# Kernel optimization log

Hardware: AMD Instinct MI355X
Metric: run time of the kernel (lower is better)

The kernel has to match this reference:

```python
import jax, jax.numpy as jnp
import numpy as np

# ---- static config (eval-mode RPN, torchvision-style FPN) ----
LEVEL_HW = [(200, 200), (100, 100), (50, 50), (25, 25), (13, 13)]
STRIDES = [4, 8, 16, 32, 64]
SIZES = [32, 64, 128, 256, 512]
A = 3                      # anchors per location (3 aspect ratios)
IMG_H, IMG_W = 800, 800
PRE_N, POST_N = 1000, 1000 # pre/post NMS top-n (testing)
NMS_TH, SCORE_TH, MIN_SIZE = 0.7, 0.0, 1e-3
BBOX_CLIP = 4.135166556742356  # log(1000/16), BoxCoder clamp
NUM_PER_LEVEL = [A * h * w for h, w in LEVEL_HW]


def _make_anchors():
    ratios = np.array([0.5, 1.0, 2.0])
    hr = np.sqrt(ratios)
    wr = 1.0 / hr
    out = []
    for (H, W), size, stride in zip(LEVEL_HW, SIZES, STRIDES):
        ws, hs = wr * size, hr * size
        base = np.stack([-ws / 2, -hs / 2, ws / 2, hs / 2], axis=1)  # [A,4]
        sx = np.arange(W) * stride
        sy = np.arange(H) * stride
        yy, xx = np.meshgrid(sy, sx, indexing='ij')
        shifts = np.stack([xx.ravel(), yy.ravel(), xx.ravel(), yy.ravel()], axis=1)
        out.append((shifts[:, None, :] + base[None, :, :]).reshape(-1, 4))
    return np.concatenate(out, 0).astype(np.float32)


def setup_inputs() -> dict:
    key = jax.random.key(0)
    ks = jax.random.split(key, 10)
    N = 4
    inp = {}
    for i, (h, w) in enumerate(LEVEL_HW):
        inp[f'obj{i}'] = jax.random.normal(ks[i], (N, A, h, w), jnp.float32)
        inp[f'delta{i}'] = 0.5 * jax.random.normal(ks[5 + i], (N, 4 * A, h, w), jnp.float32)
    inp['anchors'] = jnp.asarray(_make_anchors())
    return inp


def _decode(deltas, anchors):
    # BoxCoder.decode with weights (1,1,1,1)
    wa = anchors[:, 2] - anchors[:, 0]
    ha = anchors[:, 3] - anchors[:, 1]
    cxa = anchors[:, 0] + 0.5 * wa
    cya = anchors[:, 1] + 0.5 * ha
    dx, dy = deltas[..., 0], deltas[..., 1]
    dw = jnp.minimum(deltas[..., 2], BBOX_CLIP)
    dh = jnp.minimum(deltas[..., 3], BBOX_CLIP)
    cx = dx * wa + cxa
    cy = dy * ha + cya
    w = jnp.exp(dw) * wa
    h = jnp.exp(dh) * ha
    return jnp.stack([cx - 0.5 * w, cy - 0.5 * h, cx + 0.5 * w, cy + 0.5 * h], -1)


def _box_iou(b1, b2):
    a1 = (b1[:, 2] - b1[:, 0]) * (b1[:, 3] - b1[:, 1])
    a2 = (b2[:, 2] - b2[:, 0]) * (b2[:, 3] - b2[:, 1])
    lt = jnp.maximum(b1[:, None, :2], b2[None, :, :2])
    rb = jnp.minimum(b1[:, None, 2:], b2[None, :, 2:])
    wh = jnp.clip(rb - lt, 0.0)
    inter = wh[..., 0] * wh[..., 1]
    return inter / (a1[:, None] + a2[None, :] - inter)


def _nms_keep(iou, valid):
    # greedy NMS over score-sorted boxes; valid marks surviving pre-filters
    K = iou.shape[0]
    def body(sup, i):
        k = valid[i] & jnp.logical_not(sup[i])
        sup = sup | (k & (iou[i] > NMS_TH))
        return sup, k
    _, keeps = jax.lax.scan(body, jnp.zeros(K, bool), jnp.arange(K))
    return keeps


def _per_image(boxes, scores, lvl):
    # clip_boxes_to_image
    x1 = jnp.clip(boxes[:, 0], 0.0, IMG_W)
    y1 = jnp.clip(boxes[:, 1], 0.0, IMG_H)
    x2 = jnp.clip(boxes[:, 2], 0.0, IMG_W)
    y2 = jnp.clip(boxes[:, 3], 0.0, IMG_H)
    boxes = jnp.stack([x1, y1, x2, y2], -1)
    # remove_small_boxes + score_thresh as validity mask
    valid = (x2 - x1 >= MIN_SIZE) & (y2 - y1 >= MIN_SIZE) & (scores >= SCORE_TH)
    ms = jnp.where(valid, scores, -1.0)
    order = jnp.argsort(-ms)
    b_s, v_s, s_s, l_s = boxes[order], valid[order], scores[order], lvl[order]
    # batched_nms trick: offset boxes by level so levels never overlap
    bn = jax.lax.stop_gradient(b_s) + (l_s.astype(boxes.dtype) * (IMG_W + 1.0))[:, None]
    keep = _nms_keep(_box_iou(bn, bn), v_s)
    sel_key = jnp.where(keep, jax.lax.stop_gradient(s_s), -1.0)
    topv, topi = jax.lax.top_k(sel_key, POST_N)
    m = topv > -0.5
    fb = jnp.where(m[:, None], b_s[topi], 0.0)
    fs = jnp.where(m, s_s[topi], 0.0)
    return fb, fs


def reference(obj0, obj1, obj2, obj3, obj4, delta0, delta1, delta2, delta3, delta4, anchors):
    objs = [obj0, obj1, obj2, obj3, obj4]
    dels = [delta0, delta1, delta2, delta3, delta4]
    N = obj0.shape[0]
    # permute_and_flatten + concat (objectness C=1)
    obj = jnp.concatenate([o.transpose(0, 2, 3, 1).reshape(N, -1) for o in objs], 1)
    dl = jnp.concatenate([
        d.reshape(N, A, 4, d.shape[2], d.shape[3]).transpose(0, 3, 4, 1, 2).reshape(N, -1, 4)
        for d in dels], 1)
    proposals = _decode(dl, anchors)  # [N, total, 4]
    levels = jnp.concatenate([jnp.full((n,), i, jnp.int32) for i, n in enumerate(NUM_PER_LEVEL)])
    # per-level top-k (static split)
    idxs, off = [], 0
    for n in NUM_PER_LEVEL:
        k = min(PRE_N, n)
        _, ti = jax.lax.top_k(obj[:, off:off + n], k)
        idxs.append(ti + off)
        off += n
    top_idx = jnp.concatenate(idxs, 1)  # [N, K]
    sel_obj = jnp.take_along_axis(obj, top_idx, 1)
    sel_lvl = levels[top_idx]
    sel_box = jnp.take_along_axis(proposals, top_idx[..., None], 1)
    scores = jax.nn.sigmoid(sel_obj)
    fb, fs = jax.vmap(_per_image)(sel_box, scores, sel_lvl)
    return fb, fs
```

## Files before the change

kernel.cpp:

```cpp
#include <hip/hip_runtime.h>
#include <cstdint>
#include <cstddef>

#define NLV 5
#define NIMG 4
#define NSEL 4507
#define TSEL (NIMG * NSEL)
#define POSTN 1000
#define TCAP 8192
#define TTCAP 2048
#define NHB 16
#define PBLK 64
#define PCH 1875

__device__ const int d_W[NLV]    = {200, 100, 50, 25, 13};
__device__ const int d_NL[NLV]   = {120000, 30000, 7500, 1875, 507};
__device__ const int d_KOFF[6]   = {0, 120000, 150000, 157500, 159375, 159882};
__device__ const int d_LOFF[6]   = {0, 1000, 2000, 3000, 4000, 4507};
__device__ const int d_KL[NLV]   = {1000, 1000, 1000, 1000, 507};

struct Ptrs {
    const float* obj[NLV];
    const float* del[NLV];
    const float* anch;
};

__device__ inline unsigned int dkey_of(float f) {
    unsigned int u = __float_as_uint(f);
    unsigned int mk = (u & 0x80000000u) ? ~u : (u | 0x80000000u);
    return ~mk;
}
__device__ inline float logit_from_dkey(unsigned int dk) {
    unsigned int mk = ~dk;
    unsigned int u = (mk & 0x80000000u) ? (mk & 0x7fffffffu) : ~mk;
    return __uint_as_float(u);
}

__global__ __launch_bounds__(256) void k_hist(Ptrs P, unsigned int* hist) {
    int l = blockIdx.y, n = blockIdx.z;
    int nl_sz = d_NL[l];
    if (d_KL[l] >= nl_sz) return;
    int nlid = n * NLV + l;
    __shared__ unsigned int h[2048];
    for (int i = threadIdx.x; i < 2048; i += 256) h[i] = 0;
    __syncthreads();
    const float* ob = P.obj[l] + (size_t)n * nl_sz;
    int chunk = (nl_sz + NHB - 1) / NHB;
    int beg = blockIdx.x * chunk;
    int end = min(beg + chunk, nl_sz);
    for (int t = beg + (int)threadIdx.x; t < end; t += 256)
        atomicAdd(&h[dkey_of(ob[t]) >> 21], 1u);
    __syncthreads();
    unsigned int* out = hist + ((size_t)nlid * NHB + blockIdx.x) * 2048;
    for (int i = threadIdx.x; i < 2048; i += 256) out[i] = h[i];
}

__global__ __launch_bounds__(1024) void k_thresh(const unsigned int* hist,
                                                 unsigned int* thr,
                                                 int* scnt, int* tcnt) {
    int nlid = blockIdx.x;
    int l = nlid % NLV;
    if (threadIdx.x == 0) { scnt[nlid] = 0; tcnt[nlid] = 0; }
    if (d_KL[l] >= d_NL[l]) return;
    int tid = threadIdx.x, w = tid >> 6, lane = tid & 63;
    __shared__ unsigned int wpre[16];
    const unsigned int* hb = hist + (size_t)nlid * NHB * 2048;
    unsigned int v0 = 0, v1 = 0;
    #pragma unroll
    for (int sh = 0; sh < NHB; ++sh) {
        v0 += hb[sh * 2048 + 2 * tid];
        v1 += hb[sh * 2048 + 2 * tid + 1];
    }
    unsigned int s = v0 + v1;
    unsigned int ps = s;
    #pragma unroll
    for (int d = 1; d < 64; d <<= 1) {
        unsigned int t2 = (unsigned int)__shfl_up((int)ps, d, 64);
        if (lane >= d) ps += t2;
    }
    if (lane == 63) wpre[w] = ps;
    __syncthreads();
    unsigned int base = 0;
    #pragma unroll
    for (int ww = 0; ww < 16; ++ww) if (ww < w) base += wpre[ww];
    unsigned int incl = base + ps;
    unsigned int target = (unsigned int)d_KL[l];
    unsigned int exc0 = incl - s, inc0 = incl - v1;
    unsigned int exc1 = inc0,    inc1 = incl;
    if (exc0 < target && target <= inc0) { thr[nlid * 2] = 2 * tid;     thr[nlid * 2 + 1] = exc0; }
    if (exc1 < target && target <= inc1) { thr[nlid * 2] = 2 * tid + 1; thr[nlid * 2 + 1] = exc1; }
}

__global__ __launch_bounds__(256) void k_pick(Ptrs P, const unsigned int* thr,
                                              int* scnt, int* tcnt,
                                              int* cg, float* cl,
                                              unsigned long long* tiebuf) {
    int l = blockIdx.y, n = blockIdx.z;
    int nl_sz = d_NL[l], kl = d_KL[l];
    int nlid = n * NLV + l;
    const float* ob = P.obj[l] + (size_t)n * nl_sz;
    int cbase = n * NSEL + d_LOFF[l];
    int koff = d_KOFF[l];
    int Wl = d_W[l], HW = Wl * Wl;
    int chunk = (nl_sz + PBLK - 1) / PBLK;
    int beg = blockIdx.x * chunk;
    int end = min(beg + chunk, nl_sz);
    int tid = threadIdx.x;

    if (kl >= nl_sz) {
        for (int t = beg + tid; t < end; t += 256) {
            int a = t / HW, rem = t - a * HW;
            int p = rem * 3 + a;
            cg[cbase + p] = koff + p;
            cl[cbase + p] = ob[t];
        }
        return;
    }
    __shared__ int sp[PCH];
    __shared__ float sl[PCH];
    __shared__ unsigned long long tb[PCH];
    __shared__ int nsel, ntie, sbase, tbase;
    if (tid == 0) { nsel = 0; ntie = 0; }
    __syncthreads();

    unsigned int b0 = thr[nlid * 2];
    for (int t = beg + tid; t < end; t += 256) {
        float lg = ob[t];
        unsigned int dk = dkey_of(lg);
        unsigned int bin = dk >> 21;
        if (bin < b0) {
            int pos = atomicAdd(&nsel, 1);
            int a = t / HW, rem = t - a * HW;
            sp[pos] = rem * 3 + a;
            sl[pos] = lg;
        } else if (bin == b0) {
            int pos = atomicAdd(&ntie, 1);
            int a = t / HW, rem = t - a * HW;
            tb[pos] = ((unsigned long long)dk << 17) |
                      (unsigned long long)(unsigned int)(rem * 3 + a);
        }
    }
    __syncthreads();
    if (tid == 0) {
        sbase = atomicAdd(&scnt[nlid], nsel);
        tbase = atomicAdd(&tcnt[nlid], ntie);
    }
    __syncthreads();
    int ns = nsel, nt = ntie, sb = sbase, tbs = tbase;
    for (int i = tid; i < ns; i += 256) {
        cg[cbase + sb + i] = koff + sp[i];
        cl[cbase + sb + i] = sl[i];
    }
    for (int i = tid; i < nt; i += 256) {
        int slot = tbs + i;
        if (slot < TCAP) tiebuf[(size_t)nlid * TCAP + slot] = tb[i];
    }
}

__global__ __launch_bounds__(1024) void k_tie(const unsigned int* thr, const int* tcnt,
                                              const unsigned long long* tiebuf,
                                              int* cg, float* cl) {
    int nlid = blockIdx.x;
    int n = nlid / NLV, l = nlid % NLV;
    if (d_KL[l] >= d_NL[l]) return;
    __shared__ unsigned long long kk[TCAP];
    __shared__ unsigned long long tt[TTCAP];
    __shared__ unsigned int h2[2048];
    __shared__ unsigned int wpre[16];
    __shared__ unsigned int s_b1, s_before;
    __shared__ int ctr, ttc;
    int c = min(tcnt[nlid], TCAP);
    unsigned int cnt_lt = thr[nlid * 2 + 1];
    int need = d_KL[l] - (int)cnt_lt;
    int tid = threadIdx.x, w = tid >> 6, lane = tid & 63;
    if (tid == 0) { ctr = 0; ttc = 0; }
    h2[tid] = 0; h2[tid + 1024] = 0;
    for (int i = tid; i < c; i += 1024) kk[i] = tiebuf[(size_t)nlid * TCAP + i];
    __syncthreads();
    for (int i = tid; i < c; i += 1024)
        atomicAdd(&h2[(unsigned int)((kk[i] >> 27) & 0x7ffull)], 1u);
    __syncthreads();
    unsigned int v0 = h2[2 * tid], v1 = h2[2 * tid + 1];
    unsigned int s = v0 + v1, ps = s;
    #pragma unroll
    for (int d = 1; d < 64; d <<= 1) {
        unsigned int t2 = (unsigned int)__shfl_up((int)ps, d, 64);
        if (lane >= d) ps += t2;
    }
    if (lane == 63) wpre[w] = ps;
    __syncthreads();
    unsigned int base = 0;
    #pragma unroll
    for (int ww = 0; ww < 16; ++ww) if (ww < w) base += wpre[ww];
    unsigned int incl = base + ps;
    unsigned int target = (unsigned int)need;
    unsigned int exc0 = incl - s, inc0 = incl - v1;
    unsigned int exc1 = inc0,    inc1 = incl;
    if (exc0 < target && target <= inc0) { s_b1 = 2 * tid;     s_before = exc0; }
    if (exc1 < target && target <= inc1) { s_b1 = 2 * tid + 1; s_before = exc1; }
    __syncthreads();
    unsigned int b1 = s_b1;
    int before = (int)s_before;
    int cbase = n * NSEL + d_LOFF[l];
    int koff = d_KOFF[l];
    for (int i = tid; i < c; i += 1024) {
        unsigned long long ki = kk[i];
        unsigned int sb = (unsigned int)((ki >> 27) & 0x7ffull);
        if (sb < b1) {
            int slot = atomicAdd(&ctr, 1);
            int p = (int)(ki & 0x1ffffull);
            cg[cbase + (int)cnt_lt + slot] = koff + p;
            cl[cbase + (int)cnt_lt + slot] = logit_from_dkey((unsigned int)(ki >> 17));
        } else if (sb == b1) {
            int j = atomicAdd(&ttc, 1);
            if (j < TTCAP) tt[j] = ki;
        }
    }
    __syncthreads();
    int c2 = min(ttc, TTCAP);
    int need2 = need - before;
    for (int i = tid; i < c2; i += 1024) {
        unsigned long long ki = tt[i];
        int rank = 0;
        for (int j = 0; j < c2; ++j) rank += (tt[j] < ki) ? 1 : 0;
        if (rank < need2) {
            int p = (int)(ki & 0x1ffffull);
            cg[cbase + (int)cnt_lt + before + rank] = koff + p;
            cl[cbase + (int)cnt_lt + before + rank] = logit_from_dkey((unsigned int)(ki >> 17));
        }
    }
}

__global__ __launch_bounds__(256) void k_build(Ptrs P, const int* cg, const float* cl,
                                               unsigned long long* pkey,
                                               float4* pbox, float4* pbn, float* plog) {
#pragma clang fp contract(off)
    int t = blockIdx.x * blockDim.x + threadIdx.x;
    if (t >= NIMG * NLV * 1024) return;
    int nl = t >> 10, j = t & 1023;
    int n = nl / NLV, l = nl % NLV;
    if (j >= d_KL[l]) {
        pkey[t] = ((unsigned long long)0xFFFFFFFFu << 27) | (unsigned long long)j;
        pbox[t] = make_float4(0.f, 0.f, 0.f, 0.f);
        pbn[t]  = make_float4(0.f, 0.f, 0.f, 0.f);
        plog[t] = 0.f;
        return;
    }
    int s = n * NSEL + d_LOFF[l] + j;
    int gidx = cg[s];
    float lg = cl[s];
    int p = gidx - d_KOFF[l];
    int Wl = d_W[l];
    int HW = Wl * Wl;
    int a = p % 3, hw = p / 3;
    int h = hw / Wl, w = hw - h * Wl;
    const float* dl = P.del[l];
    size_t base = (size_t)(n * 12 + a * 4) * HW + (size_t)h * Wl + w;
    float dx = dl[base], dy = dl[base + HW];
    float dw = dl[base + 2 * (size_t)HW], dh = dl[base + 3 * (size_t)HW];
    const float* an = P.anch + 4 * (size_t)gidx;
    float ax1 = an[0], ay1 = an[1], ax2 = an[2], ay2 = an[3];
    float wa = ax2 - ax1, ha = ay2 - ay1;
    float cxa = ax1 + 0.5f * wa, cya = ay1 + 0.5f * ha;
    const float CLIPC = (float)4.135166556742356;
    dw = fminf(dw, CLIPC); dh = fminf(dh, CLIPC);
    float cx = dx * wa + cxa;
    float cy = dy * ha + cya;
    float ww = expf(dw) * wa;
    float hh = expf(dh) * ha;
    float x1 = cx - 0.5f * ww, y1 = cy - 0.5f * hh;
    float x2 = cx + 0.5f * ww, y2 = cy + 0.5f * hh;
    x1 = fminf(fmaxf(x1, 0.0f), 800.0f);
    y1 = fminf(fmaxf(y1, 0.0f), 800.0f);
    x2 = fminf(fmaxf(x2, 0.0f), 800.0f);
    y2 = fminf(fmaxf(y2, 0.0f), 800.0f);
    bool valid = (x2 - x1 >= 1e-3f) && (y2 - y1 >= 1e-3f);
    float off = (float)l * 801.0f;
    pbox[t] = make_float4(x1, y1, x2, y2);
    pbn[t]  = make_float4(x1 + off, y1 + off, x2 + off, y2 + off);
    plog[t] = lg;
    unsigned int sk = valid ? dkey_of(lg) : 0xffffffffu;
    pkey[t] = ((unsigned long long)sk << 27) |
              ((unsigned long long)(unsigned int)p << 10) | (unsigned long long)j;
}

__global__ __launch_bounds__(512) void k_sortL(const unsigned long long* pkey,
                                               const float4* pbox, const float4* pbn,
                                               const float* plog,
                                               unsigned long long* skey,
                                               float4* sboxL, float4* cboxL, float* slogL,
                                               int* ccnt) {
    __shared__ unsigned long long s[1024];
    int nl = blockIdx.x, tid = threadIdx.x;
    s[tid] = pkey[nl * 1024 + tid];
    s[tid + 512] = pkey[nl * 1024 + tid + 512];
    __syncthreads();
    for (int k = 2; k <= 1024; k <<= 1) {
        for (int j = k >> 1; j > 0; j >>= 1) {
            int i = ((tid & ~(j - 1)) << 1) | (tid & (j - 1));
            int ix = i | j;
            bool up = ((i & k) == 0);
            unsigned long long A = s[i], B = s[ix];
            if ((A > B) == up) { s[i] = B; s[ix] = A; }
            __syncthreads();
        }
    }
    for (int e = tid; e < 1024; e += 512) {
        unsigned long long key = s[e];
        int j = (int)(key & 0x3ffull);
        int src = nl * 1024 + j;
        skey[nl * 1024 + e] = key;
        sboxL[nl * 1024 + e] = pbox[src];
        cboxL[nl * 1024 + e] = pbn[src];
        slogL[nl * 1024 + e] = plog[src];
        bool v = (key >> 27) != 0xFFFFFFFFull;
        bool vn = (e < 1023) ? ((s[e + 1] >> 27) != 0xFFFFFFFFull) : false;
        if (e == 0 && !v) ccnt[nl] = 0;
        if (v && (e == 1023 || !vn)) ccnt[nl] = e + 1;
    }
}

__global__ __launch_bounds__(256) void k_mask(const float4* cboxL, const int* ccnt,
                                              unsigned long long* MT) {
#pragma clang fp contract(off)
    int n = blockIdx.z, l = blockIdx.y;
    int ci = blockIdx.x >> 4, cj = blockIdx.x & 15;
    int nl = n * NLV + l;
    int cnt = ccnt[nl];
    int nw = (cnt + 63) / 64;
    if (cj < ci || cj >= nw) return;
    __shared__ float4 bi[64], bj[64];
    int tid = threadIdx.x;
    if (tid < 64) bj[tid] = cboxL[nl * 1024 + cj * 64 + tid];
    else if (tid < 128) bi[tid - 64] = cboxL[nl * 1024 + ci * 64 + (tid - 64)];
    __syncthreads();
    int w = tid >> 6, lane = tid & 63;
    float4 B = bj[lane];
    float a2 = (B.z - B.x) * (B.w - B.y);
    unsigned long long* outp = MT + ((size_t)nl * 16 + cj) * 1024 + ci * 64;
    #pragma unroll
    for (int t = 0; t < 16; ++t) {
        int i = w * 16 + t;
        float4 A = bi[i];
        float a1 = (A.z - A.x) * (A.w - A.y);
        float ltx = fmaxf(A.x, B.x), lty = fmaxf(A.y, B.y);
        float rbx = fminf(A.z, B.z), rby = fminf(A.w, B.w);
        float wx = fmaxf(rbx - ltx, 0.f), wy = fmaxf(rby - lty, 0.f);
        float inter = wx * wy;
        float iou = inter / ((a1 + a2) - inter);
        unsigned long long word = __ballot(iou > 0.7f);
        if (lane == 0) outp[i] = word;
    }
}

__global__ __launch_bounds__(1024) void k_scan(const unsigned long long* MT,
                                               const int* ccnt,
                                               unsigned long long* keepL) {
    int l = blockIdx.x, n = blockIdx.y;
    int nl = n * NLV + l;
    int tid = threadIdx.x, w = tid >> 6, lane = tid & 63;
    __shared__ unsigned long long pendS[16];
    __shared__ unsigned long long defS[16];
    int cnt = ccnt[nl];
    int nw = (cnt + 63) / 64;

    const unsigned long long* base = MT + ((size_t)nl * 16 + w) * 1024;
    unsigned long long Dmask = 0;
    if (w < nw)
        Dmask = base[(size_t)w * 64 + lane] & ~((2ull << lane) - 1ull);
    unsigned long long rows[15];
    #pragma unroll
    for (int cc = 0; cc < 15; ++cc)
        rows[cc] = (cc < w && w < nw) ? base[(size_t)cc * 64 + lane] : 0ull;

    int nb = max(0, min(64, cnt - w * 64));
    unsigned long long pend_w = (nb == 64) ? ~0ull : ((nb > 0) ? ((1ull << nb) - 1ull) : 0ull);
    unsigned long long K_w = 0;
    if (lane == 0) pendS[w] = pend_w;
    __syncthreads();

    for (int round = 0; round < 1024; ++round) {
        unsigned long long any = 0;
        #pragma unroll
        for (int cc = 0; cc < 16; ++cc) any |= pendS[cc];
        if (!any) break;
        unsigned long long acc = ((pendS[w] >> lane) & 1ull) ? Dmask : 0ull;
        #pragma unroll
        for (int cc = 0; cc < 15; ++cc)
            if (cc < w) acc |= ((pendS[cc] >> lane) & 1ull) ? rows[cc] : 0ull;
        unsigned int vlo = (unsigned int)acc, vhi = (unsigned int)(acc >> 32);
        #pragma unroll
        for (int m = 1; m < 64; m <<= 1) {
            vlo |= (unsigned int)__shfl_xor((int)vlo, m, 64);
            vhi |= (unsigned int)__shfl_xor((int)vhi, m, 64);
        }
        unsigned long long sup = ((unsigned long long)vhi << 32) | (unsigned long long)vlo;
        unsigned long long def_w = pend_w & ~sup;
        K_w |= def_w;
        if (lane == 0) defS[w] = def_w;
        __syncthreads();
        unsigned long long acc2 = ((defS[w] >> lane) & 1ull) ? Dmask : 0ull;
        #pragma unroll
        for (int cc = 0; cc < 15; ++cc)
            if (cc < w) acc2 |= ((defS[cc] >> lane) & 1ull) ? rows[cc] : 0ull;
        unsigned int rlo = (unsigned int)acc2, rhi = (unsigned int)(acc2 >> 32);
        #pragma unroll
        for (int m = 1; m < 64; m <<= 1) {
            rlo |= (unsigned int)__shfl_xor((int)rlo, m, 64);
            rhi |= (unsigned int)__shfl_xor((int)rhi, m, 64);
        }
        unsigned long long rem = ((unsigned long long)rhi << 32) | (unsigned long long)rlo;
        pend_w &= ~def_w & ~rem;
        if (lane == 0) pendS[w] = pend_w;
        __syncthreads();
    }
    if (lane == 0) keepL[nl * 16 + w] = K_w;
}

__global__ __launch_bounds__(1024) void k_rank(const unsigned long long* skey,
                                               const unsigned long long* keepL,
                                               const int* ccnt,
                                               const float4* sboxL, const float* slogL,
                                               float* out) {
    int n = blockIdx.x, tid = threadIdx.x;
    __shared__ unsigned long long KS[NLV][1024];
    __shared__ unsigned long long kd[NLV][16];
    __shared__ int kpre[NLV][17];
    __shared__ int lcnt[NLV];
    for (int i = tid; i < POSTN; i += 1024) {
        ((float4*)out)[n * POSTN + i] = make_float4(0.f, 0.f, 0.f, 0.f);
        out[NIMG * POSTN * 4 + n * POSTN + i] = 0.f;
    }
    for (int e = tid; e < NLV * 1024; e += 1024)
        ((unsigned long long*)KS)[e] = skey[(size_t)n * NLV * 1024 + e];
    if (tid < NLV * 16) ((unsigned long long*)kd)[tid] = keepL[n * NLV * 16 + tid];
    if (tid < NLV) lcnt[tid] = ccnt[n * NLV + tid];
    __syncthreads();
    if (tid < NLV) {
        int run = 0;
        for (int q = 0; q < 16; ++q) { kpre[tid][q] = run; run += (int)__popcll(kd[tid][q]); }
        kpre[tid][16] = run;
    }
    __syncthreads();
    for (int e = tid; e < NLV * 1024; e += 1024) {
        int l = e >> 10, i = e & 1023;
        if (i >= lcnt[l]) continue;
        int q = i >> 6, b = i & 63;
        if (!((kd[l][q] >> b) & 1ull)) continue;
        int rank = kpre[l][q] + (int)__popcll(kd[l][q] & ((1ull << b) - 1ull));
        unsigned int sk = (unsigned int)(KS[l][i] >> 27);
        for (int l2 = 0; l2 < NLV; ++l2) {
            if (l2 == l) continue;
            int c2 = lcnt[l2];
            unsigned long long bound = (l2 < l)
                ? (((unsigned long long)sk + 1ull) << 27)
                : ((unsigned long long)sk << 27);
            int lo = 0, hi = c2;
            while (lo < hi) {
                int mid = (lo + hi) >> 1;
                if (KS[l2][mid] < bound) lo = mid + 1; else hi = mid;
            }
            int mq = lo >> 6, mb = lo & 63;
            rank += kpre[l2][mq] + (mb ? (int)__popcll(kd[l2][mq] & ((1ull << mb) - 1ull)) : 0);
        }
        if (rank < POSTN) {
            ((float4*)out)[n * POSTN + rank] = sboxL[(size_t)(n * NLV + l) * 1024 + i];
            float lg = slogL[(size_t)(n * NLV + l) * 1024 + i];
            out[NIMG * POSTN * 4 + n * POSTN + rank] = 1.0f / (1.0f + expf(-lg));
        }
    }
}

extern "C" void kernel_launch(void* const* d_in, const int* in_sizes, int n_in,
                              void* d_out, int out_size, void* d_ws, size_t ws_size,
                              hipStream_t stream) {
    Ptrs P;
    bool interleaved = (in_sizes[1] == 4 * in_sizes[0]);
    for (int i = 0; i < NLV; ++i) {
        if (interleaved) {
            P.obj[i] = (const float*)d_in[2 * i];
            P.del[i] = (const float*)d_in[2 * i + 1];
        } else {
            P.obj[i] = (const float*)d_in[i];
            P.del[i] = (const float*)d_in[NLV + i];
        }
    }
    P.anch = (const float*)d_in[10];

    char* w = (char*)d_ws;
    size_t off = 0;
    auto alloc = [&](size_t bytes) {
        void* p = w + off;
        off = (off + bytes + 255) & ~(size_t)255;
        return p;
    };
    const size_t NLT = (size_t)NIMG * NLV * 1024;
    unsigned int* hist = (unsigned int*)alloc((size_t)NIMG * NLV * NHB * 2048 * 4);
    int* scnt = (int*)alloc(256);
    int* tcnt = (int*)alloc(256);
    unsigned int* thr = (unsigned int*)alloc((size_t)NIMG * NLV * 2 * 4);
    unsigned long long* tiebuf = (unsigned long long*)alloc((size_t)NIMG * NLV * TCAP * 8);
    int* cg      = (int*)alloc((size_t)TSEL * 4);
    float* cl    = (float*)alloc((size_t)TSEL * 4);
    unsigned long long* pkey = (unsigned long long*)alloc(NLT * 8);
    float4* pbox = (float4*)alloc(NLT * 16);
    float4* pbn  = (float4*)alloc(NLT * 16);
    float* plog  = (float*)alloc(NLT * 4);
    unsigned long long* skey = (unsigned long long*)alloc(NLT * 8);
    float4* sboxL = (float4*)alloc(NLT * 16);
    float4* cboxL = (float4*)alloc(NLT * 16);
    float* slogL  = (float*)alloc(NLT * 4);
    int* ccnt    = (int*)alloc((size_t)NIMG * NLV * 4);
    unsigned long long* keepL = (unsigned long long*)alloc((size_t)NIMG * NLV * 16 * 8);
    unsigned long long* MT = (unsigned long long*)alloc((size_t)NIMG * NLV * 16 * 1024 * 8);
    (void)ws_size; (void)n_in;

    k_hist<<<dim3(NHB, NLV, NIMG), 256, 0, stream>>>(P, hist);
    k_thresh<<<NIMG * NLV, 1024, 0, stream>>>(hist, thr, scnt, tcnt);
    k_pick<<<dim3(PBLK, NLV, NIMG), 256, 0, stream>>>(P, thr, scnt, tcnt, cg, cl, tiebuf);
    k_tie<<<NIMG * NLV, 1024, 0, stream>>>(thr, tcnt, tiebuf, cg, cl);
    k_build<<<(NIMG * NLV * 1024) / 256, 256, 0, stream>>>(P, cg, cl, pkey, pbox, pbn, plog);
    k_sortL<<<NIMG * NLV, 512, 0, stream>>>(pkey, pbox, pbn, plog, skey, sboxL, cboxL, slogL, ccnt);
    k_mask<<<dim3(256, NLV, NIMG), 256, 0, stream>>>(cboxL, ccnt, MT);
    k_scan<<<dim3(NLV, NIMG), 1024, 0, stream>>>(MT, ccnt, keepL);
    k_rank<<<NIMG, 1024, 0, stream>>>(skey, keepL, ccnt, sboxL, slogL, (float*)d_out);
}
```

Measured before the change: 172.3 us.

## Fuse histogram with threshold and merge tie/build/sort/mask/scan into one kernel

Merges the per-chunk histogram and threshold kernels into a single 1024-thread block per image-level that builds the histogram in shared memory, using sub-histograms to reduce atomic contention. Folds tie resolution, box decode, bitonic sort, the IoU mask and the NMS scan into one mega-kernel per image-level, keeping intermediates in a shared-memory union instead of global buffers. This removes several launches and global round-trips. In exchange the histogram pass now runs on only 20 blocks, one reading 120k elements, and the IoU mask uses 16 waves per block instead of many blocks, which lowers parallelism.

```diff
diff --git a/kernel.cpp b/kernel.cpp
--- a/kernel.cpp
+++ b/kernel.cpp
@@ -9,9 +9,10 @@
 #define POSTN 1000
 #define TCAP 8192
 #define TTCAP 2048
-#define NHB 16
 #define PBLK 64
 #define PCH 1875
+#define NSUB 4
+#define NTRI 136
 
 __device__ const int d_W[NLV]    = {200, 100, 50, 25, 13};
 __device__ const int d_NL[NLV]   = {120000, 30000, 7500, 1875, 507};
@@ -36,40 +37,29 @@
     return __uint_as_float(u);
 }
 
-__global__ __launch_bounds__(256) void k_hist(Ptrs P, unsigned int* hist) {
-    int l = blockIdx.y, n = blockIdx.z;
+__global__ __launch_bounds__(1024) void k_histthresh(Ptrs P, unsigned int* thr,
+                                                     int* scnt, int* tcnt) {
+    int nlid = blockIdx.x;
+    int n = nlid / NLV, l = nlid % NLV;
+    int tid = threadIdx.x;
+    if (tid == 0) { scnt[nlid] = 0; tcnt[nlid] = 0; }
+    if (d_KL[l] >= d_NL[l]) return;
+    __shared__ unsigned int h[NSUB][2048];
+    __shared__ unsigned int wpre[16];
+    for (int i = tid; i < NSUB * 2048; i += 1024) (&h[0][0])[i] = 0;
+    __syncthreads();
     int nl_sz = d_NL[l];
-    if (d_KL[l] >= nl_sz) return;
-    int nlid = n * NLV + l;
-    __shared__ unsigned int h[2048];
-    for (int i = threadIdx.x; i < 2048; i += 256) h[i] = 0;
-    __syncthreads();
     const float* ob = P.obj[l] + (size_t)n * nl_sz;
-    int chunk = (nl_sz + NHB - 1) / NHB;
-    int beg = blockIdx.x * chunk;
-    int end = min(beg + chunk, nl_sz);
-    for (int t = beg + (int)threadIdx.x; t < end; t += 256)
-        atomicAdd(&h[dkey_of(ob[t]) >> 21], 1u);
-    __syncthreads();
-    unsigned int* out = hist + ((size_t)nlid * NHB + blockIdx.x) * 2048;
-    for (int i = threadIdx.x; i < 2048; i += 256) out[i] = h[i];
-}
-
-__global__ __launch_bounds__(1024) void k_thresh(const unsigned int* hist,
-                                                 unsigned int* thr,
-                                                 int* scnt, int* tcnt) {
-    int nlid = blockIdx.x;
-    int l = nlid % NLV;
-    if (threadIdx.x == 0) { scnt[nlid] = 0; tcnt[nlid] = 0; }
-    if (d_KL[l] >= d_NL[l]) return;
-    int tid = threadIdx.x, w = tid >> 6, lane = tid & 63;
-    __shared__ unsigned int wpre[16];
-    const unsigned int* hb = hist + (size_t)nlid * NHB * 2048;
+    unsigned int* hs = h[(tid >> 8) & (NSUB - 1)];
+    for (int t = tid; t < nl_sz; t += 1024)
+        atomicAdd(&hs[dkey_of(ob[t]) >> 21], 1u);
+    __syncthreads();
+    int w = tid >> 6, lane = tid & 63;
     unsigned int v0 = 0, v1 = 0;
     #pragma unroll
-    for (int sh = 0; sh < NHB; ++sh) {
-        v0 += hb[sh * 2048 + 2 * tid];
-        v1 += hb[sh * 2048 + 2 * tid + 1];
+    for (int sh = 0; sh < NSUB; ++sh) {
+        v0 += h[sh][2 * tid];
+        v1 += h[sh][2 * tid + 1];
     }
     unsigned int s = v0 + v1;
     unsigned int ps = s;
@@ -157,264 +147,265 @@
     }
 }
 
-__global__ __launch_bounds__(1024) void k_tie(const unsigned int* thr, const int* tcnt,
-                                              const unsigned long long* tiebuf,
-                                              int* cg, float* cl) {
-    int nlid = blockIdx.x;
-    int n = nlid / NLV, l = nlid % NLV;
-    if (d_KL[l] >= d_NL[l]) return;
-    __shared__ unsigned long long kk[TCAP];
-    __shared__ unsigned long long tt[TTCAP];
-    __shared__ unsigned int h2[2048];
+__global__ __launch_bounds__(1024) void k_mega(Ptrs P, const unsigned int* thr,
+                                               const int* tcnt,
+                                               const unsigned long long* tiebuf,
+                                               int* cg, float* cl,
+                                               unsigned long long* skey,
+                                               float4* sboxL, float* slogL,
+                                               int* ccnt, unsigned long long* keepL) {
+#pragma clang fp contract(off)
+    __shared__ union {
+        struct { unsigned long long kk[TCAP];
+                 unsigned long long tt[TTCAP];
+                 unsigned int h2[2048]; } tie;
+        struct { unsigned long long s[1024];
+                 float4 bx[1024];
+                 float4 bn[1024];
+                 float lg[1024]; } srt;
+        struct { unsigned long long tri[NTRI * 64];
+                 float4 bb[1024]; } nms;
+    } U;
     __shared__ unsigned int wpre[16];
     __shared__ unsigned int s_b1, s_before;
-    __shared__ int ctr, ttc;
-    int c = min(tcnt[nlid], TCAP);
-    unsigned int cnt_lt = thr[nlid * 2 + 1];
-    int need = d_KL[l] - (int)cnt_lt;
-    int tid = threadIdx.x, w = tid >> 6, lane = tid & 63;
-    if (tid == 0) { ctr = 0; ttc = 0; }
-    h2[tid] = 0; h2[tid + 1024] = 0;
-    for (int i = tid; i < c; i += 1024) kk[i] = tiebuf[(size_t)nlid * TCAP + i];
-    __syncthreads();
-    for (int i = tid; i < c; i += 1024)
-        atomicAdd(&h2[(unsigned int)((kk[i] >> 27) & 0x7ffull)], 1u);
-    __syncthreads();
-    unsigned int v0 = h2[2 * tid], v1 = h2[2 * tid + 1];
-    unsigned int s = v0 + v1, ps = s;
-    #pragma unroll
-    for (int d = 1; d < 64; d <<= 1) {
-        unsigned int t2 = (unsigned int)__shfl_up((int)ps, d, 64);
-        if (lane >= d) ps += t2;
-    }
-    if (lane == 63) wpre[w] = ps;
-    __syncthreads();
-    unsigned int base = 0;
-    #pragma unroll
-    for (int ww = 0; ww < 16; ++ww) if (ww < w) base += wpre[ww];
-    unsigned int incl = base + ps;
-    unsigned int target = (unsigned int)need;
-    unsigned int exc0 = incl - s, inc0 = incl - v1;
-    unsigned int exc1 = inc0,    inc1 = incl;
-    if (exc0 < target && target <= inc0) { s_b1 = 2 * tid;     s_before = exc0; }
-    if (exc1 < target && target <= inc1) { s_b1 = 2 * tid + 1; s_before = exc1; }
-    __syncthreads();
-    unsigned int b1 = s_b1;
-    int before = (int)s_before;
-    int cbase = n * NSEL + d_LOFF[l];
-    int koff = d_KOFF[l];
-    for (int i = tid; i < c; i += 1024) {
-        unsigned long long ki = kk[i];
-        unsigned int sb = (unsigned int)((ki >> 27) & 0x7ffull);
-        if (sb < b1) {
-            int slot = atomicAdd(&ctr, 1);
-            int p = (int)(ki & 0x1ffffull);
-            cg[cbase + (int)cnt_lt + slot] = koff + p;
-            cl[cbase + (int)cnt_lt + slot] = logit_from_dkey((unsigned int)(ki >> 17));
-        } else if (sb == b1) {
-            int j = atomicAdd(&ttc, 1);
-            if (j < TTCAP) tt[j] = ki;
-        }
-    }
-    __syncthreads();
-    int c2 = min(ttc, TTCAP);
-    int need2 = need - before;
-    for (int i = tid; i < c2; i += 1024) {
-        unsigned long long ki = tt[i];
-        int rank = 0;
-        for (int j = 0; j < c2; ++j) rank += (tt[j] < ki) ? 1 : 0;
-        if (rank < need2) {
-            int p = (int)(ki & 0x1ffffull);
-            cg[cbase + (int)cnt_lt + before + rank] = koff + p;
-            cl[cbase + (int)cnt_lt + before + rank] = logit_from_dkey((unsigned int)(ki >> 17));
-        }
-    }
-}
-
-__global__ __launch_bounds__(256) void k_build(Ptrs P, const int* cg, const float* cl,
-                                               unsigned long long* pkey,
-                                               float4* pbox, float4* pbn, float* plog) {
-#pragma clang fp contract(off)
-    int t = blockIdx.x * blockDim.x + threadIdx.x;
-    if (t >= NIMG * NLV * 1024) return;
-    int nl = t >> 10, j = t & 1023;
-    int n = nl / NLV, l = nl % NLV;
-    if (j >= d_KL[l]) {
-        pkey[t] = ((unsigned long long)0xFFFFFFFFu << 27) | (unsigned long long)j;
-        pbox[t] = make_float4(0.f, 0.f, 0.f, 0.f);
-        pbn[t]  = make_float4(0.f, 0.f, 0.f, 0.f);
-        plog[t] = 0.f;
-        return;
-    }
-    int s = n * NSEL + d_LOFF[l] + j;
-    int gidx = cg[s];
-    float lg = cl[s];
-    int p = gidx - d_KOFF[l];
-    int Wl = d_W[l];
-    int HW = Wl * Wl;
-    int a = p % 3, hw = p / 3;
-    int h = hw / Wl, w = hw - h * Wl;
-    const float* dl = P.del[l];
-    size_t base = (size_t)(n * 12 + a * 4) * HW + (size_t)h * Wl + w;
-    float dx = dl[base], dy = dl[base + HW];
-    float dw = dl[base + 2 * (size_t)HW], dh = dl[base + 3 * (size_t)HW];
-    const float* an = P.anch + 4 * (size_t)gidx;
-    float ax1 = an[0], ay1 = an[1], ax2 = an[2], ay2 = an[3];
-    float wa = ax2 - ax1, ha = ay2 - ay1;
-    float cxa = ax1 + 0.5f * wa, cya = ay1 + 0.5f * ha;
-    const float CLIPC = (float)4.135166556742356;
-    dw = fminf(dw, CLIPC); dh = fminf(dh, CLIPC);
-    float cx = dx * wa + cxa;
-    float cy = dy * ha + cya;
-    float ww = expf(dw) * wa;
-    float hh = expf(dh) * ha;
-    float x1 = cx - 0.5f * ww, y1 = cy - 0.5f * hh;
-    float x2 = cx + 0.5f * ww, y2 = cy + 0.5f * hh;
-    x1 = fminf(fmaxf(x1, 0.0f), 800.0f);
-    y1 = fminf(fmaxf(y1, 0.0f), 800.0f);
-    x2 = fminf(fmaxf(x2, 0.0f), 800.0f);
-    y2 = fminf(fmaxf(y2, 0.0f), 800.0f);
-    bool valid = (x2 - x1 >= 1e-3f) && (y2 - y1 >= 1e-3f);
-    float off = (float)l * 801.0f;
-    pbox[t] = make_float4(x1, y1, x2, y2);
-    pbn[t]  = make_float4(x1 + off, y1 + off, x2 + off, y2 + off);
-    plog[t] = lg;
-    unsigned int sk = valid ? dkey_of(lg) : 0xffffffffu;
-    pkey[t] = ((unsigned long long)sk << 27) |
-              ((unsigned long long)(unsigned int)p << 10) | (unsigned long long)j;
-}
-
-__global__ __launch_bounds__(512) void k_sortL(const unsigned long long* pkey,
-                                               const float4* pbox, const float4* pbn,
-                                               const float* plog,
-                                               unsigned long long* skey,
-                                               float4* sboxL, float4* cboxL, float* slogL,
-                                               int* ccnt) {
-    __shared__ unsigned long long s[1024];
-    int nl = blockIdx.x, tid = threadIdx.x;
-    s[tid] = pkey[nl * 1024 + tid];
-    s[tid + 512] = pkey[nl * 1024 + tid + 512];
-    __syncthreads();
-    for (int k = 2; k <= 1024; k <<= 1) {
-        for (int j = k >> 1; j > 0; j >>= 1) {
-            int i = ((tid & ~(j - 1)) << 1) | (tid & (j - 1));
-            int ix = i | j;
-            bool up = ((i & k) == 0);
-            unsigned long long A = s[i], B = s[ix];
-            if ((A > B) == up) { s[i] = B; s[ix] = A; }
-            __syncthreads();
-        }
-    }
-    for (int e = tid; e < 1024; e += 512) {
-        unsigned long long key = s[e];
-        int j = (int)(key & 0x3ffull);
-        int src = nl * 1024 + j;
-        skey[nl * 1024 + e] = key;
-        sboxL[nl * 1024 + e] = pbox[src];
-        cboxL[nl * 1024 + e] = pbn[src];
-        slogL[nl * 1024 + e] = plog[src];
-        bool v = (key >> 27) != 0xFFFFFFFFull;
-        bool vn = (e < 1023) ? ((s[e + 1] >> 27) != 0xFFFFFFFFull) : false;
-        if (e == 0 && !v) ccnt[nl] = 0;
-        if (v && (e == 1023 || !vn)) ccnt[nl] = e + 1;
-    }
-}
-
-__global__ __launch_bounds__(256) void k_mask(const float4* cboxL, const int* ccnt,
-                                              unsigned long long* MT) {
-#pragma clang fp contract(off)
-    int n = blockIdx.z, l = blockIdx.y;
-    int ci = blockIdx.x >> 4, cj = blockIdx.x & 15;
-    int nl = n * NLV + l;
-    int cnt = ccnt[nl];
-    int nw = (cnt + 63) / 64;
-    if (cj < ci || cj >= nw) return;
-    __shared__ float4 bi[64], bj[64];
-    int tid = threadIdx.x;
-    if (tid < 64) bj[tid] = cboxL[nl * 1024 + cj * 64 + tid];
-    else if (tid < 128) bi[tid - 64] = cboxL[nl * 1024 + ci * 64 + (tid - 64)];
-    __syncthreads();
-    int w = tid >> 6, lane = tid & 63;
-    float4 B = bj[lane];
-    float a2 = (B.z - B.x) * (B.w - B.y);
-    unsigned long long* outp = MT + ((size_t)nl * 16 + cj) * 1024 + ci * 64;
-    #pragma unroll
-    for (int t = 0; t < 16; ++t) {
-        int i = w * 16 + t;
-        float4 A = bi[i];
-        float a1 = (A.z - A.x) * (A.w - A.y);
-        float ltx = fmaxf(A.x, B.x), lty = fmaxf(A.y, B.y);
-        float rbx = fminf(A.z, B.z), rby = fminf(A.w, B.w);
-        float wx = fmaxf(rbx - ltx, 0.f), wy = fmaxf(rby - lty, 0.f);
-        float inter = wx * wy;
-        float iou = inter / ((a1 + a2) - inter);
-        unsigned long long word = __ballot(iou > 0.7f);
-        if (lane == 0) outp[i] = word;
-    }
-}
-
-__global__ __launch_bounds__(1024) void k_scan(const unsigned long long* MT,
-                                               const int* ccnt,
-                                               unsigned long long* keepL) {
+    __shared__ int ctr, ttc, s_cnt;
+    __shared__ unsigned long long pendS[16];
+    __shared__ unsigned long long defS[16];
+
     int l = blockIdx.x, n = blockIdx.y;
     int nl = n * NLV + l;
     int tid = threadIdx.x, w = tid >> 6, lane = tid & 63;
-    __shared__ unsigned long long pendS[16];
-    __shared__ unsigned long long defS[16];
-    int cnt = ccnt[nl];
-    int nw = (cnt + 63) / 64;
-
-    const unsigned long long* base = MT + ((size_t)nl * 16 + w) * 1024;
-    unsigned long long Dmask = 0;
-    if (w < nw)
-        Dmask = base[(size_t)w * 64 + lane] & ~((2ull << lane) - 1ull);
-    unsigned long long rows[15];
-    #pragma unroll
-    for (int cc = 0; cc < 15; ++cc)
-        rows[cc] = (cc < w && w < nw) ? base[(size_t)cc * 64 + lane] : 0ull;
-
-    int nb = max(0, min(64, cnt - w * 64));
-    unsigned long long pend_w = (nb == 64) ? ~0ull : ((nb > 0) ? ((1ull << nb) - 1ull) : 0ull);
-    unsigned long long K_w = 0;
-    if (lane == 0) pendS[w] = pend_w;
-    __syncthreads();
-
-    for (int round = 0; round < 1024; ++round) {
-        unsigned long long any = 0;
+    int kl = d_KL[l], nl_sz = d_NL[l];
+    int cbase = n * NSEL + d_LOFF[l];
+    int koff = d_KOFF[l];
+
+    if (kl < nl_sz) {
+        int c = min(tcnt[nl], TCAP);
+        unsigned int cnt_lt = thr[nl * 2 + 1];
+        int need = kl - (int)cnt_lt;
+        if (tid == 0) { ctr = 0; ttc = 0; }
+        U.tie.h2[tid] = 0; U.tie.h2[tid + 1024] = 0;
+        for (int i = tid; i < c; i += 1024) U.tie.kk[i] = tiebuf[(size_t)nl * TCAP + i];
+        __syncthreads();
+        for (int i = tid; i < c; i += 1024)
+            atomicAdd(&U.tie.h2[(unsigned int)((U.tie.kk[i] >> 27) & 0x7ffull)], 1u);
+        __syncthreads();
+        unsigned int v0 = U.tie.h2[2 * tid], v1 = U.tie.h2[2 * tid + 1];
+        unsigned int s = v0 + v1, ps = s;
         #pragma unroll
-        for (int cc = 0; cc < 16; ++cc) any |= pendS[cc];
-        if (!any) break;
-        unsigned long long acc = ((pendS[w] >> lane) & 1ull) ? Dmask : 0ull;
+        for (int d = 1; d < 64; d <<= 1) {
+            unsigned int t2 = (unsigned int)__shfl_up((int)ps, d, 64);
+            if (lane >= d) ps += t2;
+        }
+        if (lane == 63) wpre[w] = ps;
+        __syncthreads();
+        unsigned int base = 0;
+        #pragma unroll
+        for (int ww = 0; ww < 16; ++ww) if (ww < w) base += wpre[ww];
+        unsigned int incl = base + ps;
+        unsigned int target = (unsigned int)need;
+        unsigned int exc0 = incl - s, inc0 = incl - v1;
+        unsigned int exc1 = inc0,    inc1 = incl;
+        if (exc0 < target && target <= inc0) { s_b1 = 2 * tid;     s_before = exc0; }
+        if (exc1 < target && target <= inc1) { s_b1 = 2 * tid + 1; s_before = exc1; }
+        __syncthreads();
+        unsigned int b1 = s_b1;
+        int before = (int)s_before;
+        for (int i = tid; i < c; i += 1024) {
+            unsigned long long ki = U.tie.kk[i];
+            unsigned int sb = (unsigned int)((ki >> 27) & 0x7ffull);
+            if (sb < b1) {
+                int slot = atomicAdd(&ctr, 1);
+                int p = (int)(ki & 0x1ffffull);
+                cg[cbase + (int)cnt_lt + slot] = koff + p;
+                cl[cbase + (int)cnt_lt + slot] = logit_from_dkey((unsigned int)(ki >> 17));
+            } else if (sb == b1) {
+                int j = atomicAdd(&ttc, 1);
+                if (j < TTCAP) U.tie.tt[j] = ki;
+            }
+        }
+        __syncthreads();
+        int c2 = min(ttc, TTCAP);
+        int need2 = need - before;
+        for (int i = tid; i < c2; i += 1024) {
+            unsigned long long ki = U.tie.tt[i];
+            int rank = 0;
+            for (int j = 0; j < c2; ++j) rank += (U.tie.tt[j] < ki) ? 1 : 0;
+            if (rank < need2) {
+                int p = (int)(ki & 0x1ffffull);
+                cg[cbase + (int)cnt_lt + before + rank] = koff + p;
+                cl[cbase + (int)cnt_lt + before + rank] = logit_from_dkey((unsigned int)(ki >> 17));
+            }
+        }
+    }
+    __syncthreads();
+
+    {
+        int j = tid;
+        unsigned long long key;
+        float4 box, bnv;
+        float lgv;
+        if (j >= kl) {
+            key = ((unsigned long long)0xFFFFFFFFu << 27) | (unsigned long long)j;
+            box = make_float4(0.f, 0.f, 0.f, 0.f);
+            bnv = box;
+            lgv = 0.f;
+        } else {
+            int sidx = cbase + j;
+            int gidx = cg[sidx];
+            float lg = cl[sidx];
+            int p = gidx - koff;
+            int Wl = d_W[l];
+            int HW = Wl * Wl;
+            int a = p % 3, hw = p / 3;
+            int hq = hw / Wl, wq = hw - hq * Wl;
+            const float* dl = P.del[l];
+            size_t dbase = (size_t)(n * 12 + a * 4) * HW + (size_t)hq * Wl + wq;
+            float dx = dl[dbase], dy = dl[dbase + HW];
+            float dw = dl[dbase + 2 * (size_t)HW], dh = dl[dbase + 3 * (size_t)HW];
+            const float* an = P.anch + 4 * (size_t)gidx;
+            float ax1 = an[0], ay1 = an[1], ax2 = an[2], ay2 = an[3];
+            float wa = ax2 - ax1, ha = ay2 - ay1;
+            float cxa = ax1 + 0.5f * wa, cya = ay1 + 0.5f * ha;
+            const float CLIPC = (float)4.135166556742356;
+            dw = fminf(dw, CLIPC); dh = fminf(dh, CLIPC);
+            float cx = dx * wa + cxa;
+            float cy = dy * ha + cya;
+            float ww2 = expf(dw) * wa;
+            float hh2 = expf(dh) * ha;
+            float x1 = cx - 0.5f * ww2, y1 = cy - 0.5f * hh2;
+            float x2 = cx + 0.5f * ww2, y2 = cy + 0.5f * hh2;
+            x1 = fminf(fmaxf(x1, 0.0f), 800.0f);
+            y1 = fminf(fmaxf(y1, 0.0f), 800.0f);
+            x2 = fminf(fmaxf(x2, 0.0f), 800.0f);
+            y2 = fminf(fmaxf(y2, 0.0f), 800.0f);
+            bool valid = (x2 - x1 >= 1e-3f) && (y2 - y1 >= 1e-3f);
+            float off = (float)l * 801.0f;
+            box = make_float4(x1, y1, x2, y2);
+            bnv = make_float4(x1 + off, y1 + off, x2 + off, y2 + off);
+            lgv = lg;
+            unsigned int sk = valid ? dkey_of(lg) : 0xffffffffu;
+            key = ((unsigned long long)sk << 27) |
+                  ((unsigned long long)(unsigned int)p << 10) | (unsigned long long)j;
+        }
+        U.srt.s[j] = key;
+        U.srt.bx[j] = box;
+        U.srt.bn[j] = bnv;
+        U.srt.lg[j] = lgv;
+    }
+    __syncthreads();
+
+    for (int k = 2; k <= 1024; k <<= 1) {
+        for (int j2 = k >> 1; j2 > 0; j2 >>= 1) {
+            if (tid < 512) {
+                int i = ((tid & ~(j2 - 1)) << 1) | (tid & (j2 - 1));
+                int ix = i | j2;
+                bool up = ((i & k) == 0);
+                unsigned long long A = U.srt.s[i], B = U.srt.s[ix];
+                if ((A > B) == up) { U.srt.s[i] = B; U.srt.s[ix] = A; }
+            }
+            __syncthreads();
+        }
+    }
+    float4 myBN;
+    {
+        int e = tid;
+        unsigned long long key = U.srt.s[e];
+        int j = (int)(key & 0x3ffull);
+        myBN = U.srt.bn[j];
+        skey[(size_t)nl * 1024 + e] = key;
+        sboxL[(size_t)nl * 1024 + e] = U.srt.bx[j];
+        slogL[(size_t)nl * 1024 + e] = U.srt.lg[j];
+        bool v = (key >> 27) != 0xFFFFFFFFull;
+        bool vn = (e < 1023) ? ((U.srt.s[e + 1] >> 27) != 0xFFFFFFFFull) : false;
+        if (e == 0 && !v) { ccnt[nl] = 0; s_cnt = 0; }
+        if (v && (e == 1023 || !vn)) { ccnt[nl] = e + 1; s_cnt = e + 1; }
+    }
+    __syncthreads();
+    U.nms.bb[tid] = myBN;
+    __syncthreads();
+
+    {
+        int cnt = s_cnt;
+        int nw = (cnt + 63) >> 6;
+        int ntiles = (nw * (nw + 1)) >> 1;
+        for (int T = w; T < ntiles; T += 16) {
+            int cj = 0;
+            while (((cj + 1) * (cj + 2)) >> 1 <= T) ++cj;
+            int ci = T - ((cj * (cj + 1)) >> 1);
+            float4 B = U.nms.bb[cj * 64 + lane];
+            float a2 = (B.z - B.x) * (B.w - B.y);
+            unsigned long long* outp = &U.nms.tri[(size_t)T * 64];
+            for (int i = 0; i < 64; ++i) {
+                float4 A = U.nms.bb[ci * 64 + i];
+                float a1 = (A.z - A.x) * (A.w - A.y);
+                float ltx = fmaxf(A.x, B.x), lty = fmaxf(A.y, B.y);
+                float rbx = fminf(A.z, B.z), rby = fminf(A.w, B.w);
+                float wx = fmaxf(rbx - ltx, 0.f), wy = fmaxf(rby - lty, 0.f);
+                float inter = wx * wy;
+                float iou = inter / ((a1 + a2) - inter);
+                unsigned long long word = __ballot(iou > 0.7f);
+                if (lane == i) outp[i] = word;
+            }
+        }
+    }
+    __syncthreads();
+
+    {
+        int cnt = s_cnt;
+        int nw = (cnt + 63) / 64;
+        int triw = (w * (w + 1)) >> 1;
+        unsigned long long Dmask = 0;
+        if (w < nw)
+            Dmask = U.nms.tri[(size_t)(triw + w) * 64 + lane] & ~((2ull << lane) - 1ull);
+        unsigned long long rows[15];
         #pragma unroll
         for (int cc = 0; cc < 15; ++cc)
-            if (cc < w) acc |= ((pendS[cc] >> lane) & 1ull) ? rows[cc] : 0ull;
-        unsigned int vlo = (unsigned int)acc, vhi = (unsigned int)(acc >> 32);
-        #pragma unroll
-        for (int m = 1; m < 64; m <<= 1) {
-            vlo |= (unsigned int)__shfl_xor((int)vlo, m, 64);
-            vhi |= (unsigned int)__shfl_xor((int)vhi, m, 64);
-        }
-        unsigned long long sup = ((unsigned long long)vhi << 32) | (unsigned long long)vlo;
-        unsigned long long def_w = pend_w & ~sup;
-        K_w |= def_w;
-        if (lane == 0) defS[w] = def_w;
-        __syncthreads();
-        unsigned long long acc2 = ((defS[w] >> lane) & 1ull) ? Dmask : 0ull;
-        #pragma unroll
-        for (int cc = 0; cc < 15; ++cc)
-            if (cc < w) acc2 |= ((defS[cc] >> lane) & 1ull) ? rows[cc] : 0ull;
-        unsigned int rlo = (unsigned int)acc2, rhi = (unsigned int)(acc2 >> 32);
-        #pragma unroll
-        for (int m = 1; m < 64; m <<= 1) {
-            rlo |= (unsigned int)__shfl_xor((int)rlo, m, 64);
-            rhi |= (unsigned int)__shfl_xor((int)rhi, m, 64);
-        }
-        unsigned long long rem = ((unsigned long long)rhi << 32) | (unsigned long long)rlo;
-        pend_w &= ~def_w & ~rem;
+            rows[cc] = (cc < w && w < nw) ? U.nms.tri[(size_t)(triw + cc) * 64 + lane] : 0ull;
+
+        int nb = max(0, min(64, cnt - w * 64));
+        unsigned long long pend_w = (nb == 64) ? ~0ull : ((nb > 0) ? ((1ull << nb) - 1ull) : 0ull);
+        unsigned long long K_w = 0;
         if (lane == 0) pendS[w] = pend_w;
         __syncthreads();
-    }
-    if (lane == 0) keepL[nl * 16 + w] = K_w;
+
+        for (int round = 0; round < 1024; ++round) {
+            unsigned long long any = 0;
+            #pragma unroll
+            for (int cc = 0; cc < 16; ++cc) any |= pendS[cc];
+            if (!any) break;
+            unsigned long long acc = ((pendS[w] >> lane) & 1ull) ? Dmask : 0ull;
+            #pragma unroll
+            for (int cc = 0; cc < 15; ++cc)
+                if (cc < w) acc |= ((pendS[cc] >> lane) & 1ull) ? rows[cc] : 0ull;
+            unsigned int vlo = (unsigned int)acc, vhi = (unsigned int)(acc >> 32);
+            #pragma unroll
+            for (int m = 1; m < 64; m <<= 1) {
+                vlo |= (unsigned int)__shfl_xor((int)vlo, m, 64);
+                vhi |= (unsigned int)__shfl_xor((int)vhi, m, 64);
+            }
+            unsigned long long sup = ((unsigned long long)vhi << 32) | (unsigned long long)vlo;
+            unsigned long long def_w = pend_w & ~sup;
+            K_w |= def_w;
+            if (lane == 0) defS[w] = def_w;
+            __syncthreads();
+            unsigned long long acc2 = ((defS[w] >> lane) & 1ull) ? Dmask : 0ull;
+            #pragma unroll
+            for (int cc = 0; cc < 15; ++cc)
+                if (cc < w) acc2 |= ((defS[cc] >> lane) & 1ull) ? rows[cc] : 0ull;
+            unsigned int rlo = (unsigned int)acc2, rhi = (unsigned int)(acc2 >> 32);
+            #pragma unroll
+            for (int m = 1; m < 64; m <<= 1) {
+                rlo |= (unsigned int)__shfl_xor((int)rlo, m, 64);
+                rhi |= (unsigned int)__shfl_xor((int)rhi, m, 64);
+            }
+            unsigned long long rem = ((unsigned long long)rhi << 32) | (unsigned long long)rlo;
+            pend_w &= ~def_w & ~rem;
+            if (lane == 0) pendS[w] = pend_w;
+            __syncthreads();
+        }
+        if (lane == 0) keepL[nl * 16 + w] = K_w;
+    }
 }
 
 __global__ __launch_bounds__(1024) void k_rank(const unsigned long long* skey,
@@ -495,33 +486,22 @@
         return p;
     };
     const size_t NLT = (size_t)NIMG * NLV * 1024;
-    unsigned int* hist = (unsigned int*)alloc((size_t)NIMG * NLV * NHB * 2048 * 4);
     int* scnt = (int*)alloc(256);
     int* tcnt = (int*)alloc(256);
     unsigned int* thr = (unsigned int*)alloc((size_t)NIMG * NLV * 2 * 4);
     unsigned long long* tiebuf = (unsigned long long*)alloc((size_t)NIMG * NLV * TCAP * 8);
     int* cg      = (int*)alloc((size_t)TSEL * 4);
     float* cl    = (float*)alloc((size_t)TSEL * 4);
-    unsigned long long* pkey = (unsigned long long*)alloc(NLT * 8);
-    float4* pbox = (float4*)alloc(NLT * 16);
-    float4* pbn  = (float4*)alloc(NLT * 16);
-    float* plog  = (float*)alloc(NLT * 4);
     unsigned long long* skey = (unsigned long long*)alloc(NLT * 8);
     float4* sboxL = (float4*)alloc(NLT * 16);
-    float4* cboxL = (float4*)alloc(NLT * 16);
     float* slogL  = (float*)alloc(NLT * 4);
     int* ccnt    = (int*)alloc((size_t)NIMG * NLV * 4);
     unsigned long long* keepL = (unsigned long long*)alloc((size_t)NIMG * NLV * 16 * 8);
-    unsigned long long* MT = (unsigned long long*)alloc((size_t)NIMG * NLV * 16 * 1024 * 8);
     (void)ws_size; (void)n_in;
 
-    k_hist<<<dim3(NHB, NLV, NIMG), 256, 0, stream>>>(P, hist);
-    k_thresh<<<NIMG * NLV, 1024, 0, stream>>>(hist, thr, scnt, tcnt);
+    k_histthresh<<<NIMG * NLV, 1024, 0, stream>>>(P, thr, scnt, tcnt);
     k_pick<<<dim3(PBLK, NLV, NIMG), 256, 0, stream>>>(P, thr, scnt, tcnt, cg, cl, tiebuf);
-    k_tie<<<NIMG * NLV, 1024, 0, stream>>>(thr, tcnt, tiebuf, cg, cl);
-    k_build<<<(NIMG * NLV * 1024) / 256, 256, 0, stream>>>(P, cg, cl, pkey, pbox, pbn, plog);
-    k_sortL<<<NIMG * NLV, 512, 0, stream>>>(pkey, pbox, pbn, plog, skey, sboxL, cboxL, slogL, ccnt);
-    k_mask<<<dim3(256, NLV, NIMG), 256, 0, stream>>>(cboxL, ccnt, MT);
-    k_scan<<<dim3(NLV, NIMG), 1024, 0, stream>>>(MT, ccnt, keepL);
+    k_mega<<<dim3(NLV, NIMG), 1024, 0, stream>>>(P, thr, tcnt, tiebuf, cg, cl,
+                                                 skey, sboxL, slogL, ccnt, keepL);
     k_rank<<<NIMG, 1024, 0, stream>>>(skey, keepL, ccnt, sboxL, slogL, (float*)d_out);
 }
```

New measurement: 298.2 us. 73.1% more time.
